# Optimization experiments

Hardware: AMD Instinct MI355X
Metric: run time of the kernel (lower is better)

The kernel has to match this reference:

```python
import jax, jax.numpy as jnp
import numpy as np

N_NODES = 100000
N_EDGES = 1600000
N_GRAPHS = 512
EPS = 1e-12


def _glorot(key, shape):
    lim = float(np.sqrt(6.0 / (shape[0] + shape[1])))
    return jax.random.uniform(key, shape, jnp.float32, -lim, lim)


def setup_inputs() -> dict:
    key = jax.random.key(0)
    ks = jax.random.split(key, 16)
    x = jax.random.normal(ks[0], (N_NODES, 5), jnp.float32)
    edge_index = jax.random.randint(ks[1], (2, N_EDGES), 0, N_NODES)
    batch = jnp.sort(jax.random.randint(ks[2], (N_NODES,), 0, N_GRAPHS))
    return {
        "x": x,
        "edge_index": edge_index,
        "batch": batch,
        "num_graphs": N_GRAPHS,
        # pre: Linear(5, 32)
        "pre_w": _glorot(ks[3], (5, 32)), "pre_b": jnp.zeros((32,), jnp.float32),
        # conv1: SAGEConv(32, 64): lin_l (agg, bias), lin_r (root, no bias)
        "c1_wl": _glorot(ks[4], (32, 64)), "c1_bl": jnp.zeros((64,), jnp.float32),
        "c1_wr": _glorot(ks[5], (32, 64)),
        # conv2: SAGEConv(64, 64)
        "c2_wl": _glorot(ks[6], (64, 64)), "c2_bl": jnp.zeros((64,), jnp.float32),
        "c2_wr": _glorot(ks[7], (64, 64)),
        # post / out linears
        "p1_w": _glorot(ks[8], (64, 64)), "p1_b": jnp.zeros((64,), jnp.float32),
        "p2_w": _glorot(ks[9], (64, 16)), "p2_b": jnp.zeros((16,), jnp.float32),
        "o_w": _glorot(ks[10], (16, 1)), "o_b": jnp.zeros((1,), jnp.float32),
    }


def _sage_conv(x, src, dst, w_l, b_l, w_r, n_nodes):
    # mean-aggregate neighbor messages src -> dst
    msg = x[src]                                              # [E, d]
    agg = jax.ops.segment_sum(msg, dst, num_segments=n_nodes)  # [N, d]
    cnt = jax.ops.segment_sum(jnp.ones((src.shape[0], 1), x.dtype), dst,
                              num_segments=n_nodes)            # [N, 1]
    agg = jnp.where(cnt > 0, agg / jnp.maximum(cnt, 1.0), 0.0)
    out = agg @ w_l + b_l + x @ w_r
    # normalize=True -> L2 normalize per node
    nrm = jnp.linalg.norm(out, axis=-1, keepdims=True)
    return out / jnp.maximum(nrm, EPS)


def reference(x, edge_index, batch, num_graphs,
              pre_w, pre_b, c1_wl, c1_bl, c1_wr, c2_wl, c2_bl, c2_wr,
              p1_w, p1_b, p2_w, p2_b, o_w, o_b):
    n_nodes = x.shape[0]
    src, dst = edge_index[0], edge_index[1]
    h = jax.nn.relu(x @ pre_w + pre_b)
    h = jax.nn.relu(_sage_conv(h, src, dst, c1_wl, c1_bl, c1_wr, n_nodes))
    h = jax.nn.relu(_sage_conv(h, src, dst, c2_wl, c2_bl, c2_wr, n_nodes))
    # global mean pool over batch index
    s = jax.ops.segment_sum(h, batch, num_segments=num_graphs)          # [G, d]
    c = jax.ops.segment_sum(jnp.ones((n_nodes, 1), h.dtype), batch,
                            num_segments=num_graphs)                    # [G, 1]
    g = s / jnp.maximum(c, 1.0)
    g = jax.nn.relu(g @ p1_w + p1_b)
    g = jax.nn.relu(g @ p2_w + p2_b)
    out = g @ o_w + o_b
    return out.squeeze(-1)
```

## Files before the change

kernel.cpp:

```cpp
#include <hip/hip_runtime.h>

#define EPSN 1e-12f
#define TILE 2048
#define BSH 8
#define BNODES 256
#define SBMAX 512
#define BCAP 4608
#define CSRCAP 512

using frag_ab = __attribute__((ext_vector_type(8))) short;
using frag_cd = __attribute__((ext_vector_type(4))) float;
using f32x2   = __attribute__((ext_vector_type(2))) float;

template <bool B> struct BoolC { static constexpr bool value = B; };

__device__ inline unsigned short f2bf(float x) {
    union { float f; unsigned u; } v; v.f = x;
    unsigned r = v.u + 0x7fffu + ((v.u >> 16) & 1u);
    return (unsigned short)(r >> 16);
}
__device__ inline unsigned short pk2fp8(float a, float b) {
    return (unsigned short)(__builtin_amdgcn_cvt_pk_fp8_f32(a, b, 0, false) & 0xffff);
}
__device__ inline unsigned char to_fp8(float a) {
    return (unsigned char)(__builtin_amdgcn_cvt_pk_fp8_f32(a, a, 0, false) & 0xff);
}

__global__ __launch_bounds__(256) void prep_all(
    const float* __restrict__ x, const float* __restrict__ pw,
    const float* __restrict__ pb, unsigned char* __restrict__ h0, int n,
    const float* __restrict__ w1l, const float* __restrict__ w1r,
    unsigned short* __restrict__ wpk1,
    const float* __restrict__ w2l, const float* __restrict__ w2r,
    unsigned short* __restrict__ wpk2,
    float* __restrict__ sg, int gtot,
    const int* __restrict__ dst, int* __restrict__ thistT, int e,
    int nsb, int nt) {
    __shared__ int lh[SBMAX];
    int tid = threadIdx.x;
    if (blockIdx.x < nt) {
        int b = blockIdx.x;
        for (int i = tid; i < nsb; i += 256) lh[i] = 0;
        __syncthreads();
        int base = b * TILE, lim = min(base + TILE, e);
        for (int i = base + tid; i < lim; i += 256) atomicAdd(&lh[dst[i] >> BSH], 1);
        __syncthreads();
        for (int i = tid; i < nsb; i += 256) thistT[(size_t)b * nsb + i] = lh[i];
        return;
    }
    int idx = (blockIdx.x - nt) * 256 + tid;
    int npre = n * 16;
    if (idx < npre) {
        int node = idx >> 4, j2 = idx & 15;
        int j = j2 * 2;
        float v0 = pb[j], v1 = pb[j + 1];
#pragma unroll
        for (int k = 0; k < 5; ++k) {
            float xv = x[node * 5 + k];
            v0 += xv * pw[k * 32 + j];
            v1 += xv * pw[k * 32 + j + 1];
        }
        ((unsigned short*)h0)[node * 16 + j2] =
            pk2fp8(fmaxf(v0, 0.f), fmaxf(v1, 0.f));
        return;
    }
    int o = idx - npre;
    if (o < 64 * 64) {
        int j = o / 64, k = o % 64;
        float v = (k < 32) ? w1l[k * 64 + j] : w1r[(k - 32) * 64 + j];
        wpk1[o] = f2bf(v);
        return;
    }
    o -= 64 * 64;
    if (o < 64 * 128) {
        int j = o / 128, k = o % 128;
        float v = (k < 64) ? w2l[k * 64 + j] : w2r[(k - 64) * 64 + j];
        wpk2[o] = f2bf(v);
        return;
    }
    o -= 64 * 128;
    if (o < gtot) sg[o] = 0.f;
}

__global__ __launch_bounds__(256) void tscan_k(const int* __restrict__ thistT,
                                               int* __restrict__ toffsT,
                                               int* __restrict__ btot,
                                               int nsb, int nt) {
    __shared__ int wsum[8];
    int b = blockIdx.x;
    int tid = threadIdx.x;
    int lane = tid & 63, w = tid >> 6;
    int run = 0;
    for (int base = 0; base < nt; base += 256) {
        int i = base + tid;
        int x = (i < nt) ? thistT[(size_t)i * nsb + b] : 0;
        int inc = x;
#pragma unroll
        for (int o = 1; o < 64; o <<= 1) {
            int t = __shfl_up(inc, o);
            if (lane >= o) inc += t;
        }
        if (lane == 63) wsum[w] = inc;
        __syncthreads();
        if (tid == 0) {
            int s = 0;
#pragma unroll
            for (int k = 0; k < 4; ++k) { int t = wsum[k]; wsum[k] = s; s += t; }
            wsum[4] = s;
        }
        __syncthreads();
        if (i < nt) toffsT[(size_t)b * nt + i] = inc - x + wsum[w] + run;
        run += wsum[4];
        __syncthreads();
    }
    if (tid == 0) btot[b] = run;
}

__global__ __launch_bounds__(256) void scat1_k(const int* __restrict__ src,
                                               const int* __restrict__ dst,
                                               const int* __restrict__ toffsT,
                                               int* __restrict__ staged, int e,
                                               int nsb, int nt) {
    __shared__ int cur[SBMAX];
    int tid = threadIdx.x;
    for (int i = tid; i < nsb; i += 256)
        cur[i] = i * BCAP + toffsT[(size_t)i * nt + blockIdx.x];
    __syncthreads();
    int base = blockIdx.x * TILE;
    int lim = min(base + TILE, e);
    for (int i = base + tid; i < lim; i += 256) {
        int d = dst[i];
        int p = atomicAdd(&cur[d >> BSH], 1);
        staged[p] = (src[i] << BSH) | (d & (BNODES - 1));
    }
}

__global__ __launch_bounds__(256) void scat2_k(const int* __restrict__ btot,
                                               const int* __restrict__ staged,
                                               int* __restrict__ csr,
                                               int* __restrict__ rofs,
                                               int* __restrict__ deg,
                                               int n, int nsb) {
    __shared__ int h[BNODES];
    __shared__ int cur[BNODES];
    __shared__ int wsum[8];
    int b = blockIdx.x;
    int tid = threadIdx.x;
    int lane = tid & 63, w = tid >> 6;
    int nlo = b << BSH;
    int nn = n - nlo; if (nn > BNODES) nn = BNODES;
    int lo = b * BCAP, hi = lo + btot[b];
    h[tid] = 0;
    __syncthreads();
    for (int i = lo + tid; i < hi; i += 256) atomicAdd(&h[staged[i] & (BNODES - 1)], 1);
    __syncthreads();
    int x = h[tid];
    int inc = x;
#pragma unroll
    for (int o = 1; o < 64; o <<= 1) {
        int t = __shfl_up(inc, o);
        if (lane >= o) inc += t;
    }
    if (lane == 63) wsum[w] = inc;
    __syncthreads();
    if (tid == 0) {
        int s = 0;
#pragma unroll
        for (int k = 0; k < 4; ++k) { int t = wsum[k]; wsum[k] = s; s += t; }
    }
    __syncthreads();
    int excl = inc - x + wsum[w];
    cur[tid] = excl;
    if (tid < nn) {
        rofs[nlo + tid] = lo + excl;
        deg[nlo + tid] = x;
    }
    __syncthreads();
    for (int i = lo + tid; i < hi; i += 256) {
        int v = staged[i];
        int p = atomicAdd(&cur[v & (BNODES - 1)], 1);
        csr[lo + p] = v >> BSH;
    }
}

template <int KE, bool POOL>
__global__ __launch_bounds__(256) void conv_mfma(
    const int* __restrict__ rofs, const int* __restrict__ deg,
    const int* __restrict__ csr,
    const unsigned char* __restrict__ hin, const unsigned short* __restrict__ wpk,
    const float* __restrict__ bl, const int* __restrict__ batch,
    float* __restrict__ sg, unsigned char* __restrict__ hout, int n) {
    constexpr int KT = 2 * KE;
    constexpr int ST = KT + 8;
    constexpr int KS = KT / 32;
    constexpr int LPE = KE / 8;
    constexpr int EPW = 64 / LPE;
    constexpr int RB = 16 / EPW;
    __shared__ unsigned short __attribute__((aligned(16))) Ab[16 * ST];
    __shared__ float __attribute__((aligned(16))) Nb[4][16];
    __shared__ int ro[16];
    __shared__ int dg[16];
    __shared__ int sb[16];
    __shared__ int csrL[CSRCAP];

    int tid = threadIdx.x;
    int w = tid >> 6;
    int lane = tid & 63;
    int quad = lane >> 4;
    int l16 = lane & 15;
    int base = blockIdx.x * 16;
    int ncol = w * 16 + l16;

    if (tid < 16) {
        int nd = base + tid;
        bool v = nd < n;
        ro[tid] = v ? rofs[nd] : 0;
        dg[tid] = v ? deg[nd] : 0;
        if (POOL) sb[tid] = v ? batch[nd] : -1;
    }

    frag_ab bfrag[KS];
#pragma unroll
    for (int s = 0; s < KS; ++s)
        bfrag[s] = *(const frag_ab*)&wpk[(((ncol * KS) + s) * 4 + quad) * 8];
    float bias = bl[ncol];
    __syncthreads();

    int ro0 = ro[0];
    int lastv = min(15, n - 1 - base);
    int span = ro[lastv] + dg[lastv] - ro0;
    int spanL = min(span, CSRCAP);
    for (int i = tid; i < spanL; i += 256) csrL[i] = csr[ro0 + i];

    int grp = lane / LPE;
    int p = lane % LPE;
    int beg[4], cnt[4], lim[4], pcnt[4];
#pragma unroll
    for (int i = 0; i < 4; ++i) {
        int li = w * 4 + i;
        beg[i] = ro[li] - ro0;
        cnt[i] = dg[li];
        lim[i] = max(beg[i] + cnt[i] - 1, 0);
        pcnt[i] = (cnt[i] + 15) & ~15;
    }
    int msE = max(max(pcnt[0], pcnt[1]), max(pcnt[2], pcnt[3]));

    int sn = grp & 3;
    bool doAgg = grp < 4;
    bool doSelf = (grp >= 4) && (grp < 8);
    int snode = base + w * 4 + sn;
    uint2 selfv = make_uint2(0u, 0u);
    if (doSelf && snode < n)
        selfv = *(const uint2*)&hin[(size_t)snode * KE + p * 8];
    __syncthreads();

    f32x2 AL[4][4];
#pragma unroll
    for (int i = 0; i < 4; ++i)
#pragma unroll
        for (int q = 0; q < 4; ++q) AL[i][q] = (f32x2){0.f, 0.f};

    auto run_sweeps = [&](auto uselc) {
        constexpr bool USEL = decltype(uselc)::value;
        for (int e0 = 0; e0 < msE; e0 += 16) {
            uint2 u[4][RB];
#pragma unroll
            for (int i = 0; i < 4; ++i) {
                if (e0 < pcnt[i]) {
#pragma unroll
                    for (int r = 0; r < RB; ++r) {
                        int raw = beg[i] + e0 + r * EPW + grp;
                        int offc = min(raw, lim[i]);
                        int idx;
                        if (USEL) idx = csrL[offc];
                        else idx = csr[ro0 + offc];
                        u[i][r] = *(const uint2*)&hin[(size_t)idx * KE + p * 8];
                    }
                }
            }
#pragma unroll
            for (int i = 0; i < 4; ++i) {
                if (e0 < pcnt[i]) {
#pragma unroll
                    for (int r = 0; r < RB; ++r) {
                        bool ok = (e0 + r * EPW + grp) < cnt[i];
                        unsigned ux = ok ? u[i][r].x : 0u;
                        unsigned uy = ok ? u[i][r].y : 0u;
                        AL[i][0] += __builtin_amdgcn_cvt_pk_f32_fp8(ux, false);
                        AL[i][1] += __builtin_amdgcn_cvt_pk_f32_fp8(ux, true);
                        AL[i][2] += __builtin_amdgcn_cvt_pk_f32_fp8(uy, false);
                        AL[i][3] += __builtin_amdgcn_cvt_pk_f32_fp8(uy, true);
                    }
                }
            }
        }
    };
    if (span <= CSRCAP) run_sweeps(BoolC<true>{});
    else run_sweeps(BoolC<false>{});

    float A[4][8];
#pragma unroll
    for (int i = 0; i < 4; ++i) {
#pragma unroll
        for (int q = 0; q < 4; ++q) {
            A[i][2 * q] = AL[i][q].x;
            A[i][2 * q + 1] = AL[i][q].y;
        }
    }

#pragma unroll
    for (int i = 0; i < 4; ++i) {
#pragma unroll
        for (int o = LPE; o < 64; o <<= 1) {
#pragma unroll
            for (int q = 0; q < 8; ++q) A[i][q] += __shfl_xor(A[i][q], o);
        }
    }

    float av[8];
#pragma unroll
    for (int q = 0; q < 8; ++q) av[q] = A[0][q];
    int cs = cnt[0];
#pragma unroll
    for (int i = 1; i < 4; ++i) {
        bool m = (sn == i);
#pragma unroll
        for (int q = 0; q < 8; ++q) av[q] = m ? A[i][q] : av[q];
        cs = m ? cnt[i] : cs;
    }
    {
        int li = w * 4 + sn;
        int node = base + li;
        if (node < n) {
            if (doAgg) {
                float inv = (cs > 0) ? 1.0f / (float)cs : 0.0f;
                uint4 o4;
                o4.x = (unsigned)f2bf(av[0] * inv) | ((unsigned)f2bf(av[1] * inv) << 16);
                o4.y = (unsigned)f2bf(av[2] * inv) | ((unsigned)f2bf(av[3] * inv) << 16);
                o4.z = (unsigned)f2bf(av[4] * inv) | ((unsigned)f2bf(av[5] * inv) << 16);
                o4.w = (unsigned)f2bf(av[6] * inv) | ((unsigned)f2bf(av[7] * inv) << 16);
                *(uint4*)&Ab[li * ST + p * 8] = o4;
            }
            if (doSelf) {
                f32x2 s0 = __builtin_amdgcn_cvt_pk_f32_fp8(selfv.x, false);
                f32x2 s1 = __builtin_amdgcn_cvt_pk_f32_fp8(selfv.x, true);
                f32x2 s2 = __builtin_amdgcn_cvt_pk_f32_fp8(selfv.y, false);
                f32x2 s3 = __builtin_amdgcn_cvt_pk_f32_fp8(selfv.y, true);
                uint4 o4;
                o4.x = (unsigned)f2bf(s0.x) | ((unsigned)f2bf(s0.y) << 16);
                o4.y = (unsigned)f2bf(s1.x) | ((unsigned)f2bf(s1.y) << 16);
                o4.z = (unsigned)f2bf(s2.x) | ((unsigned)f2bf(s2.y) << 16);
                o4.w = (unsigned)f2bf(s3.x) | ((unsigned)f2bf(s3.y) << 16);
                *(uint4*)&Ab[li * ST + KE + p * 8] = o4;
            }
        }
    }
    __syncthreads();

    frag_cd acc = (frag_cd){0.f, 0.f, 0.f, 0.f};
#pragma unroll
    for (int s = 0; s < KS; ++s) {
        frag_ab af = *(frag_ab*)&Ab[l16 * ST + s * 32 + quad * 8];
        acc = __builtin_amdgcn_mfma_f32_16x16x32_bf16(af, bfrag[s], acc, 0, 0, 0);
    }

    float vv[4], q[4];
#pragma unroll
    for (int i = 0; i < 4; ++i) {
        float v = acc[i] + bias;
        vv[i] = v;
        q[i] = v * v;
    }
#pragma unroll
    for (int o = 1; o < 16; o <<= 1) {
#pragma unroll
        for (int i = 0; i < 4; ++i) q[i] += __shfl_xor(q[i], o);
    }
    if (l16 == 0)
        *(float4*)&Nb[w][quad * 4] = make_float4(q[0], q[1], q[2], q[3]);
    __syncthreads();

    float s0 = 0.f, s1 = 0.f, s2 = 0.f, s3 = 0.f;
#pragma unroll
    for (int ww = 0; ww < 4; ++ww) {
        float4 xq = *(const float4*)&Nb[ww][quad * 4];
        s0 += xq.x; s1 += xq.y; s2 += xq.z; s3 += xq.w;
    }
    float ss[4] = {s0, s1, s2, s3};
    float pv[4];
#pragma unroll
    for (int i = 0; i < 4; ++i) {
        float nv = fmaxf(sqrtf(ss[i]), EPSN);
        pv[i] = fmaxf(vv[i] / nv, 0.f);
    }

    if (!POOL) {
#pragma unroll
        for (int i = 0; i < 4; ++i) {
            int node = base + quad * 4 + i;
            if (node < n)
                hout[(size_t)node * 64 + ncol] = to_fp8(pv[i]);
        }
    } else {
        int g0 = sb[0];
        int g1 = sb[min(15, n - 1 - base)];
        for (int g = g0; g <= g1; ++g) {
            float s = 0.f;
#pragma unroll
            for (int i = 0; i < 4; ++i)
                if (sb[quad * 4 + i] == g) s += pv[i];
            s += __shfl_xor(s, 16);
            s += __shfl_xor(s, 32);
            if (quad == 0) atomicAdd(&sg[(size_t)g * 64 + ncol], s);
        }
    }
}

__global__ __launch_bounds__(64) void mlp_k(
    const float* __restrict__ sg, const int* __restrict__ batch, int n,
    const float* __restrict__ p1w, const float* __restrict__ p1b,
    const float* __restrict__ p2w, const float* __restrict__ p2b,
    const float* __restrict__ ow, const float* __restrict__ ob,
    float* __restrict__ out) {
    __shared__ float gmean[64];
    __shared__ float a1[64];
    __shared__ float a2[16];
    int g = blockIdx.x;
    int j = threadIdx.x;
    int lo = 0, hi = n;
    while (lo < hi) { int m = (lo + hi) >> 1; if (batch[m] < g) lo = m + 1; else hi = m; }
    int start = lo;
    hi = n;
    while (lo < hi) { int m = (lo + hi) >> 1; if (batch[m] < g + 1) lo = m + 1; else hi = m; }
    float c = (float)(lo - start);
    gmean[j] = sg[(size_t)g * 64 + j] / fmaxf(c, 1.0f);
    __syncthreads();
    float v = p1b[j];
#pragma unroll 8
    for (int k = 0; k < 64; ++k) v = fmaf(gmean[k], p1w[k * 64 + j], v);
    a1[j] = fmaxf(v, 0.f);
    __syncthreads();
    if (j < 16) {
        float v2 = p2b[j];
#pragma unroll 8
        for (int k = 0; k < 64; ++k) v2 = fmaf(a1[k], p2w[k * 16 + j], v2);
        a2[j] = fmaxf(v2, 0.f);
    }
    __syncthreads();
    if (j == 0) {
        float v3 = ob[0];
#pragma unroll
        for (int k = 0; k < 16; ++k) v3 = fmaf(a2[k], ow[k], v3);
        out[g] = v3;
    }
}

extern "C" void kernel_launch(void* const* d_in, const int* in_sizes, int n_in,
                              void* d_out, int out_size, void* d_ws, size_t ws_size,
                              hipStream_t stream) {
    const float* x     = (const float*)d_in[0];
    const int*   ei    = (const int*)d_in[1];
    const int*   batch = (const int*)d_in[2];
    const float* pre_w = (const float*)d_in[4];
    const float* pre_b = (const float*)d_in[5];
    const float* c1_wl = (const float*)d_in[6];
    const float* c1_bl = (const float*)d_in[7];
    const float* c1_wr = (const float*)d_in[8];
    const float* c2_wl = (const float*)d_in[9];
    const float* c2_bl = (const float*)d_in[10];
    const float* c2_wr = (const float*)d_in[11];
    const float* p1w   = (const float*)d_in[12];
    const float* p1b   = (const float*)d_in[13];
    const float* p2w   = (const float*)d_in[14];
    const float* p2b   = (const float*)d_in[15];
    const float* ow    = (const float*)d_in[16];
    const float* ob    = (const float*)d_in[17];

    const int N = in_sizes[0] / 5;
    const int E = in_sizes[1] / 2;
    const int G = out_size;
    const int NT = (E + TILE - 1) / TILE;
    const int NSB = (N + BNODES - 1) / BNODES;
    const int* src = ei;
    const int* dst = ei + E;

    size_t h0_bytes = (((size_t)N * 32) + 127) & ~(size_t)127;
    size_t h1_bytes = (((size_t)N * 64) + 127) & ~(size_t)127;
    unsigned char* h0u = (unsigned char*)d_ws;
    unsigned char* h1u = h0u + h0_bytes;
    unsigned short* wpk1 = (unsigned short*)(h1u + h1_bytes);
    unsigned short* wpk2 = wpk1 + 64 * 64;
    float* sg    = (float*)(wpk2 + 64 * 128);
    int* rofs    = (int*)(sg + (size_t)G * 64);
    int* deg     = rofs + N;
    int* btot    = deg + N;
    int* thistT  = btot + NSB;
    int* toffsT  = thistT + (size_t)NT * NSB;
    int* staged  = toffsT + (size_t)NSB * NT;
    int* csr     = staged + (size_t)NSB * BCAP;

    int prep_tot = N * 16 + 64 * 64 + 64 * 128 + G * 64;
    int prep_blocks = (prep_tot + 255) / 256;
    prep_all<<<NT + prep_blocks, 256, 0, stream>>>(
        x, pre_w, pre_b, h0u, N, c1_wl, c1_wr, wpk1, c2_wl, c2_wr, wpk2,
        sg, G * 64, dst, thistT, E, NSB, NT);

    tscan_k<<<NSB, 256, 0, stream>>>(thistT, toffsT, btot, NSB, NT);
    scat1_k<<<NT, 256, 0, stream>>>(src, dst, toffsT, staged, E, NSB, NT);
    scat2_k<<<NSB, 256, 0, stream>>>(btot, staged, csr, rofs, deg, N, NSB);

    conv_mfma<32, false><<<(N + 15) / 16, 256, 0, stream>>>(
        rofs, deg, csr, h0u, wpk1, c1_bl, batch, sg, h1u, N);
    conv_mfma<64, true><<<(N + 15) / 16, 256, 0, stream>>>(
        rofs, deg, csr, h1u, wpk2, c2_bl, batch, sg, nullptr, N);

    mlp_k<<<G, 64, 0, stream>>>(sg, batch, N, p1w, p1b, p2w, p2b, ow, ob,
                                (float*)d_out);
}
```

Before: 263.5 us.

## Process 32 nodes per block with 4-byte gathers and two MFMA tiles

```diff
diff --git a/kernel.cpp b/kernel.cpp
--- a/kernel.cpp
+++ b/kernel.cpp
@@ -6,7 +6,7 @@
 #define BNODES 256
 #define SBMAX 512
 #define BCAP 4608
-#define CSRCAP 512
+#define CSRCAP 1024
 
 using frag_ab = __attribute__((ext_vector_type(8))) short;
 using frag_cd = __attribute__((ext_vector_type(4))) float;
@@ -193,14 +193,18 @@
     constexpr int KT = 2 * KE;
     constexpr int ST = KT + 8;
     constexpr int KS = KT / 32;
-    constexpr int LPE = KE / 8;
+    constexpr int LPE = KE / 4;
     constexpr int EPW = 64 / LPE;
     constexpr int RB = 16 / EPW;
-    __shared__ unsigned short __attribute__((aligned(16))) Ab[16 * ST];
+    constexpr int NPW = 8;
+    constexpr int NB = 32;
+    constexpr int NPASS = NPW / EPW;
+    constexpr int LPS = KE / 8;
+    __shared__ unsigned short __attribute__((aligned(16))) Ab[NB * ST];
     __shared__ float __attribute__((aligned(16))) Nb[4][16];
-    __shared__ int ro[16];
-    __shared__ int dg[16];
-    __shared__ int sb[16];
+    __shared__ int ro[NB];
+    __shared__ int dg[NB];
+    __shared__ int sb[NB];
     __shared__ int csrL[CSRCAP];
 
     int tid = threadIdx.x;
@@ -208,210 +212,207 @@
     int lane = tid & 63;
     int quad = lane >> 4;
     int l16 = lane & 15;
-    int base = blockIdx.x * 16;
+    int base = blockIdx.x * NB;
     int ncol = w * 16 + l16;
 
-    if (tid < 16) {
+    if (tid < NB) {
         int nd = base + tid;
         bool v = nd < n;
         ro[tid] = v ? rofs[nd] : 0;
         dg[tid] = v ? deg[nd] : 0;
         if (POOL) sb[tid] = v ? batch[nd] : -1;
     }
+    __syncthreads();
+
+    int ro0 = ro[0];
+    int lastv = min(NB - 1, n - 1 - base);
+    int span = ro[lastv] + dg[lastv] - ro0;
+    int spanL = min(span, CSRCAP);
+    for (int i = tid; i < spanL; i += 256) csrL[i] = csr[ro0 + i];
+
+    int grp = lane / LPE;
+    int p = lane % LPE;
+    int beg[NPW], cnt[NPW];
+#pragma unroll
+    for (int i = 0; i < NPW; ++i) {
+        int li = w * NPW + i;
+        beg[i] = ro[li] - ro0;
+        cnt[i] = dg[li];
+    }
+    int msE = 0;
+#pragma unroll
+    for (int i = 0; i < NPW; ++i) msE = max(msE, cnt[i]);
+
+    int sn_s = lane / LPS, p_s = lane % LPS;
+    bool doSelf = sn_s < NPW;
+    int snode = base + w * NPW + sn_s;
+    uint2 selfv = make_uint2(0u, 0u);
+    if (doSelf && snode < n)
+        selfv = *(const uint2*)&hin[(size_t)snode * KE + p_s * 8];
+    __syncthreads();
+
+    f32x2 AL[NPW][2];
+#pragma unroll
+    for (int i = 0; i < NPW; ++i) { AL[i][0] = (f32x2){0.f, 0.f}; AL[i][1] = (f32x2){0.f, 0.f}; }
+
+    auto run_sweeps = [&](auto uselc) {
+        constexpr bool USEL = decltype(uselc)::value;
+        for (int e0 = 0; e0 < msE; e0 += 16) {
+            unsigned u[NPW][RB];
+#pragma unroll
+            for (int i = 0; i < NPW; ++i) {
+                if (e0 < cnt[i]) {
+#pragma unroll
+                    for (int r = 0; r < RB; ++r) {
+                        int raw = beg[i] + e0 + r * EPW + grp;
+                        int offc = min(raw, beg[i] + cnt[i] - 1);
+                        int idx;
+                        if (USEL) idx = csrL[offc];
+                        else idx = csr[ro0 + offc];
+                        u[i][r] = *(const unsigned*)&hin[(size_t)idx * KE + p * 4];
+                    }
+                }
+            }
+#pragma unroll
+            for (int i = 0; i < NPW; ++i) {
+                if (e0 < cnt[i]) {
+#pragma unroll
+                    for (int r = 0; r < RB; ++r) {
+                        bool ok = (e0 + r * EPW + grp) < cnt[i];
+                        unsigned ux = ok ? u[i][r] : 0u;
+                        AL[i][0] += __builtin_amdgcn_cvt_pk_f32_fp8(ux, false);
+                        AL[i][1] += __builtin_amdgcn_cvt_pk_f32_fp8(ux, true);
+                    }
+                }
+            }
+        }
+    };
+    if (span <= CSRCAP) run_sweeps(BoolC<true>{});
+    else run_sweeps(BoolC<false>{});
+
+    float A[NPW][4];
+#pragma unroll
+    for (int i = 0; i < NPW; ++i) {
+        A[i][0] = AL[i][0].x; A[i][1] = AL[i][0].y;
+        A[i][2] = AL[i][1].x; A[i][3] = AL[i][1].y;
+    }
+
+#pragma unroll
+    for (int i = 0; i < NPW; ++i) {
+#pragma unroll
+        for (int o = LPE; o < 64; o <<= 1) {
+#pragma unroll
+            for (int q = 0; q < 4; ++q) A[i][q] += __shfl_xor(A[i][q], o);
+        }
+    }
 
     frag_ab bfrag[KS];
 #pragma unroll
     for (int s = 0; s < KS; ++s)
         bfrag[s] = *(const frag_ab*)&wpk[(((ncol * KS) + s) * 4 + quad) * 8];
     float bias = bl[ncol];
-    __syncthreads();
-
-    int ro0 = ro[0];
-    int lastv = min(15, n - 1 - base);
-    int span = ro[lastv] + dg[lastv] - ro0;
-    int spanL = min(span, CSRCAP);
-    for (int i = tid; i < spanL; i += 256) csrL[i] = csr[ro0 + i];
-
-    int grp = lane / LPE;
-    int p = lane % LPE;
-    int beg[4], cnt[4], lim[4], pcnt[4];
-#pragma unroll
-    for (int i = 0; i < 4; ++i) {
-        int li = w * 4 + i;
-        beg[i] = ro[li] - ro0;
-        cnt[i] = dg[li];
-        lim[i] = max(beg[i] + cnt[i] - 1, 0);
-        pcnt[i] = (cnt[i] + 15) & ~15;
-    }
-    int msE = max(max(pcnt[0], pcnt[1]), max(pcnt[2], pcnt[3]));
-
-    int sn = grp & 3;
-    bool doAgg = grp < 4;
-    bool doSelf = (grp >= 4) && (grp < 8);
-    int snode = base + w * 4 + sn;
-    uint2 selfv = make_uint2(0u, 0u);
-    if (doSelf && snode < n)
-        selfv = *(const uint2*)&hin[(size_t)snode * KE + p * 8];
-    __syncthreads();
-
-    f32x2 AL[4][4];
-#pragma unroll
-    for (int i = 0; i < 4; ++i)
-#pragma unroll
-        for (int q = 0; q < 4; ++q) AL[i][q] = (f32x2){0.f, 0.f};
-
-    auto run_sweeps = [&](auto uselc) {
-        constexpr bool USEL = decltype(uselc)::value;
-        for (int e0 = 0; e0 < msE; e0 += 16) {
-            uint2 u[4][RB];
-#pragma unroll
-            for (int i = 0; i < 4; ++i) {
-                if (e0 < pcnt[i]) {
-#pragma unroll
-                    for (int r = 0; r < RB; ++r) {
-                        int raw = beg[i] + e0 + r * EPW + grp;
-                        int offc = min(raw, lim[i]);
-                        int idx;
-                        if (USEL) idx = csrL[offc];
-                        else idx = csr[ro0 + offc];
-                        u[i][r] = *(const uint2*)&hin[(size_t)idx * KE + p * 8];
-                    }
-                }
-            }
-#pragma unroll
-            for (int i = 0; i < 4; ++i) {
-                if (e0 < pcnt[i]) {
-#pragma unroll
-                    for (int r = 0; r < RB; ++r) {
-                        bool ok = (e0 + r * EPW + grp) < cnt[i];
-                        unsigned ux = ok ? u[i][r].x : 0u;
-                        unsigned uy = ok ? u[i][r].y : 0u;
-                        AL[i][0] += __builtin_amdgcn_cvt_pk_f32_fp8(ux, false);
-                        AL[i][1] += __builtin_amdgcn_cvt_pk_f32_fp8(ux, true);
-                        AL[i][2] += __builtin_amdgcn_cvt_pk_f32_fp8(uy, false);
-                        AL[i][3] += __builtin_amdgcn_cvt_pk_f32_fp8(uy, true);
-                    }
-                }
-            }
-        }
-    };
-    if (span <= CSRCAP) run_sweeps(BoolC<true>{});
-    else run_sweeps(BoolC<false>{});
-
-    float A[4][8];
-#pragma unroll
-    for (int i = 0; i < 4; ++i) {
-#pragma unroll
-        for (int q = 0; q < 4; ++q) {
-            A[i][2 * q] = AL[i][q].x;
-            A[i][2 * q + 1] = AL[i][q].y;
-        }
-    }
-
-#pragma unroll
-    for (int i = 0; i < 4; ++i) {
-#pragma unroll
-        for (int o = LPE; o < 64; o <<= 1) {
-#pragma unroll
-            for (int q = 0; q < 8; ++q) A[i][q] += __shfl_xor(A[i][q], o);
-        }
-    }
-
-    float av[8];
-#pragma unroll
-    for (int q = 0; q < 8; ++q) av[q] = A[0][q];
-    int cs = cnt[0];
-#pragma unroll
-    for (int i = 1; i < 4; ++i) {
-        bool m = (sn == i);
-#pragma unroll
-        for (int q = 0; q < 8; ++q) av[q] = m ? A[i][q] : av[q];
-        cs = m ? cnt[i] : cs;
-    }
-    {
-        int li = w * 4 + sn;
+
+#pragma unroll
+    for (int pp = 0; pp < NPASS; ++pp) {
+        float av0 = A[pp * EPW][0], av1 = A[pp * EPW][1];
+        float av2 = A[pp * EPW][2], av3 = A[pp * EPW][3];
+        int cs = cnt[pp * EPW];
+#pragma unroll
+        for (int j = 1; j < EPW; ++j) {
+            bool m = (grp == j);
+            av0 = m ? A[pp * EPW + j][0] : av0; av1 = m ? A[pp * EPW + j][1] : av1;
+            av2 = m ? A[pp * EPW + j][2] : av2; av3 = m ? A[pp * EPW + j][3] : av3;
+            cs = m ? cnt[pp * EPW + j] : cs;
+        }
+        int li = w * NPW + pp * EPW + grp;
         int node = base + li;
         if (node < n) {
-            if (doAgg) {
-                float inv = (cs > 0) ? 1.0f / (float)cs : 0.0f;
-                uint4 o4;
-                o4.x = (unsigned)f2bf(av[0] * inv) | ((unsigned)f2bf(av[1] * inv) << 16);
-                o4.y = (unsigned)f2bf(av[2] * inv) | ((unsigned)f2bf(av[3] * inv) << 16);
-                o4.z = (unsigned)f2bf(av[4] * inv) | ((unsigned)f2bf(av[5] * inv) << 16);
-                o4.w = (unsigned)f2bf(av[6] * inv) | ((unsigned)f2bf(av[7] * inv) << 16);
-                *(uint4*)&Ab[li * ST + p * 8] = o4;
+            float inv = (cs > 0) ? 1.0f / (float)cs : 0.0f;
+            uint2 o2;
+            o2.x = (unsigned)f2bf(av0 * inv) | ((unsigned)f2bf(av1 * inv) << 16);
+            o2.y = (unsigned)f2bf(av2 * inv) | ((unsigned)f2bf(av3 * inv) << 16);
+            *(uint2*)&Ab[li * ST + p * 4] = o2;
+        }
+    }
+    if (doSelf && snode < n) {
+        int li = w * NPW + sn_s;
+        f32x2 s0 = __builtin_amdgcn_cvt_pk_f32_fp8(selfv.x, false);
+        f32x2 s1 = __builtin_amdgcn_cvt_pk_f32_fp8(selfv.x, true);
+        f32x2 s2 = __builtin_amdgcn_cvt_pk_f32_fp8(selfv.y, false);
+        f32x2 s3 = __builtin_amdgcn_cvt_pk_f32_fp8(selfv.y, true);
+        uint4 o4;
+        o4.x = (unsigned)f2bf(s0.x) | ((unsigned)f2bf(s0.y) << 16);
+        o4.y = (unsigned)f2bf(s1.x) | ((unsigned)f2bf(s1.y) << 16);
+        o4.z = (unsigned)f2bf(s2.x) | ((unsigned)f2bf(s2.y) << 16);
+        o4.w = (unsigned)f2bf(s3.x) | ((unsigned)f2bf(s3.y) << 16);
+        *(uint4*)&Ab[li * ST + KE + p_s * 8] = o4;
+    }
+    __syncthreads();
+
+    frag_cd acc[2];
+#pragma unroll
+    for (int t = 0; t < 2; ++t) {
+        acc[t] = (frag_cd){0.f, 0.f, 0.f, 0.f};
+#pragma unroll
+        for (int s = 0; s < KS; ++s) {
+            frag_ab af = *(frag_ab*)&Ab[(t * 16 + l16) * ST + s * 32 + quad * 8];
+            acc[t] = __builtin_amdgcn_mfma_f32_16x16x32_bf16(af, bfrag[s], acc[t], 0, 0, 0);
+        }
+    }
+
+#pragma unroll
+    for (int t = 0; t < 2; ++t) {
+        if (t) __syncthreads();
+        float vv[4], q[4];
+#pragma unroll
+        for (int i = 0; i < 4; ++i) {
+            float v = acc[t][i] + bias;
+            vv[i] = v;
+            q[i] = v * v;
+        }
+#pragma unroll
+        for (int o = 1; o < 16; o <<= 1) {
+#pragma unroll
+            for (int i = 0; i < 4; ++i) q[i] += __shfl_xor(q[i], o);
+        }
+        if (l16 == 0)
+            *(float4*)&Nb[w][quad * 4] = make_float4(q[0], q[1], q[2], q[3]);
+        __syncthreads();
+
+        float s0 = 0.f, s1 = 0.f, s2 = 0.f, s3 = 0.f;
+#pragma unroll
+        for (int ww = 0; ww < 4; ++ww) {
+            float4 xq = *(const float4*)&Nb[ww][quad * 4];
+            s0 += xq.x; s1 += xq.y; s2 += xq.z; s3 += xq.w;
+        }
+        float ss[4] = {s0, s1, s2, s3};
+        float pv[4];
+#pragma unroll
+        for (int i = 0; i < 4; ++i) {
+            float nv = fmaxf(sqrtf(ss[i]), EPSN);
+            pv[i] = fmaxf(vv[i] / nv, 0.f);
+        }
+
+        int tbase = base + t * 16;
+        if (!POOL) {
+#pragma unroll
+            for (int i = 0; i < 4; ++i) {
+                int node = tbase + quad * 4 + i;
+                if (node < n)
+                    hout[(size_t)node * 64 + ncol] = to_fp8(pv[i]);
             }
-            if (doSelf) {
-                f32x2 s0 = __builtin_amdgcn_cvt_pk_f32_fp8(selfv.x, false);
-                f32x2 s1 = __builtin_amdgcn_cvt_pk_f32_fp8(selfv.x, true);
-                f32x2 s2 = __builtin_amdgcn_cvt_pk_f32_fp8(selfv.y, false);
-                f32x2 s3 = __builtin_amdgcn_cvt_pk_f32_fp8(selfv.y, true);
-                uint4 o4;
-                o4.x = (unsigned)f2bf(s0.x) | ((unsigned)f2bf(s0.y) << 16);
-                o4.y = (unsigned)f2bf(s1.x) | ((unsigned)f2bf(s1.y) << 16);
-                o4.z = (unsigned)f2bf(s2.x) | ((unsigned)f2bf(s2.y) << 16);
-                o4.w = (unsigned)f2bf(s3.x) | ((unsigned)f2bf(s3.y) << 16);
-                *(uint4*)&Ab[li * ST + KE + p * 8] = o4;
+        } else if (tbase < n) {
+            int g0 = sb[t * 16];
+            int g1 = sb[t * 16 + min(15, n - 1 - tbase)];
+            for (int g = g0; g <= g1; ++g) {
+                float s = 0.f;
+#pragma unroll
+                for (int i = 0; i < 4; ++i)
+                    if (sb[t * 16 + quad * 4 + i] == g) s += pv[i];
+                s += __shfl_xor(s, 16);
+                s += __shfl_xor(s, 32);
+                if (quad == 0) atomicAdd(&sg[(size_t)g * 64 + ncol], s);
             }
-        }
-    }
-    __syncthreads();
-
-    frag_cd acc = (frag_cd){0.f, 0.f, 0.f, 0.f};
-#pragma unroll
-    for (int s = 0; s < KS; ++s) {
-        frag_ab af = *(frag_ab*)&Ab[l16 * ST + s * 32 + quad * 8];
-        acc = __builtin_amdgcn_mfma_f32_16x16x32_bf16(af, bfrag[s], acc, 0, 0, 0);
-    }
-
-    float vv[4], q[4];
-#pragma unroll
-    for (int i = 0; i < 4; ++i) {
-        float v = acc[i] + bias;
-        vv[i] = v;
-        q[i] = v * v;
-    }
-#pragma unroll
-    for (int o = 1; o < 16; o <<= 1) {
-#pragma unroll
-        for (int i = 0; i < 4; ++i) q[i] += __shfl_xor(q[i], o);
-    }
-    if (l16 == 0)
-        *(float4*)&Nb[w][quad * 4] = make_float4(q[0], q[1], q[2], q[3]);
-    __syncthreads();
-
-    float s0 = 0.f, s1 = 0.f, s2 = 0.f, s3 = 0.f;
-#pragma unroll
-    for (int ww = 0; ww < 4; ++ww) {
-        float4 xq = *(const float4*)&Nb[ww][quad * 4];
-        s0 += xq.x; s1 += xq.y; s2 += xq.z; s3 += xq.w;
-    }
-    float ss[4] = {s0, s1, s2, s3};
-    float pv[4];
-#pragma unroll
-    for (int i = 0; i < 4; ++i) {
-        float nv = fmaxf(sqrtf(ss[i]), EPSN);
-        pv[i] = fmaxf(vv[i] / nv, 0.f);
-    }
-
-    if (!POOL) {
-#pragma unroll
-        for (int i = 0; i < 4; ++i) {
-            int node = base + quad * 4 + i;
-            if (node < n)
-                hout[(size_t)node * 64 + ncol] = to_fp8(pv[i]);
-        }
-    } else {
-        int g0 = sb[0];
-        int g1 = sb[min(15, n - 1 - base)];
-        for (int g = g0; g <= g1; ++g) {
-            float s = 0.f;
-#pragma unroll
-            for (int i = 0; i < 4; ++i)
-                if (sb[quad * 4 + i] == g) s += pv[i];
-            s += __shfl_xor(s, 16);
-            s += __shfl_xor(s, 32);
-            if (quad == 0) atomicAdd(&sg[(size_t)g * 64 + ncol], s);
         }
     }
 }
@@ -509,9 +510,9 @@
     scat1_k<<<NT, 256, 0, stream>>>(src, dst, toffsT, staged, E, NSB, NT);
     scat2_k<<<NSB, 256, 0, stream>>>(btot, staged, csr, rofs, deg, N, NSB);
 
-    conv_mfma<32, false><<<(N + 15) / 16, 256, 0, stream>>>(
+    conv_mfma<32, false><<<(N + 31) / 32, 256, 0, stream>>>(
         rofs, deg, csr, h0u, wpk1, c1_bl, batch, sg, h1u, N);
-    conv_mfma<64, true><<<(N + 15) / 16, 256, 0, stream>>>(
+    conv_mfma<64, true><<<(N + 31) / 32, 256, 0, stream>>>(
         rofs, deg, csr, h1u, wpk2, c2_bl, batch, sg, nullptr, N);
 
     mlp_k<<<G, 64, 0, stream>>>(sg, batch, N, p1w, p1b, p2w, p2b, ow, ob,
```

Result: faster. 243.8 us (-7.5%).
